# Optimization experiments

Measured on AMD Instinct MI355X. Metric: run time of the kernel, lower is better.

The kernel has to match this reference:

```python
import jax, jax.numpy as jnp
import numpy as np

EPS = 1.1920929e-07  # torch nn.RMSNorm default eps = finfo(fp32).eps
H, NOPE, ROPE, VD = 16, 128, 64, 128
QKD = NOPE + ROPE


def rmsnorm(x, w):
    return x * jax.lax.rsqrt(jnp.mean(x * x, axis=-1, keepdims=True) + EPS) * w


def rope(x, cos, sin):
    # x: [B,S,h,D]; cos/sin broadcast to [B,S,h,D//2]; pairs are (even, odd) interleaved
    x2 = x.reshape(*x.shape[:-1], -1, 2)
    x0, x1 = x2[..., 0], x2[..., 1]
    r = x0 * cos - x1 * sin
    i = x0 * sin + x1 * cos
    return jnp.stack([r, i], axis=-1).reshape(x.shape)


def setup_inputs() -> dict:
    key = jax.random.key(0)
    ks = jax.random.split(key, 8)
    B, S, D = 2, 2048, 2048
    QR, KR = 1536, 512
    x = jax.random.normal(ks[0], (B, S, D), jnp.float32)
    # RoPE table: theta=10000, rope dim 64 -> 32 frequencies
    pos = np.arange(S)[:, None]
    inv = 1.0 / (10000.0 ** (np.arange(0, ROPE, 2) / ROPE))[None, :]
    ang = pos * inv
    freqs_cos = jnp.asarray(np.cos(ang), jnp.float32)
    freqs_sin = jnp.asarray(np.sin(ang), jnp.float32)

    def w(k, out_dim, in_dim):
        return jax.random.normal(k, (out_dim, in_dim), jnp.float32) / np.sqrt(in_dim)

    return {
        "x": x,
        "freqs_cos": freqs_cos,
        "freqs_sin": freqs_sin,
        "Wq_down": w(ks[1], QR, D),
        "q_norm_w": jnp.ones((QR,), jnp.float32),
        "Wq_up": w(ks[2], H * QKD, QR),
        "Wkv_down": w(ks[3], ROPE + KR, D),
        "kv_norm_w": jnp.ones((KR,), jnp.float32),
        "Wkv_up": w(ks[4], H * (VD + NOPE), KR),
        "Wo": w(ks[5], D, H * VD),
        "bo": jnp.zeros((D,), jnp.float32),
        "start_pos": 0,
    }


def reference(x, freqs_cos, freqs_sin, Wq_down, q_norm_w, Wq_up, Wkv_down, kv_norm_w, Wkv_up, Wo, bo, start_pos):
    B, S, D = x.shape
    cos = freqs_cos[None, :, None, :]
    sin = freqs_sin[None, :, None, :]
    # low-rank Q path: down -> RMSNorm -> up
    q = rmsnorm(x @ Wq_down.T, q_norm_w) @ Wq_up.T
    q = q.reshape(B, S, H, QKD)
    q_nope, q_rope = q[..., :NOPE], q[..., NOPE:]
    q_rope = rope(q_rope, cos, sin)
    q = jnp.concatenate([q_nope, q_rope], axis=-1)  # [B,S,H,QKD]
    # low-rank KV path: shared rope part + latent kv
    kv = x @ Wkv_down.T
    k_rope, c_kv = kv[..., :ROPE], kv[..., ROPE:]
    k_rope = rope(k_rope[:, :, None, :], cos, sin)  # [B,S,1,ROPE]
    kv = rmsnorm(c_kv, kv_norm_w) @ Wkv_up.T
    kv = kv.reshape(B, S, H, NOPE + VD)
    k_nope, v = kv[..., :NOPE], kv[..., NOPE:]
    k = jnp.concatenate([k_nope, jnp.broadcast_to(k_rope, (B, S, H, ROPE))], axis=-1)
    # causal SDPA (start_pos=0 prefill: cache slice equals fresh K/V)
    scale = 1.0 / np.sqrt(QKD)
    scores = jnp.einsum("bqhd,bkhd->bhqk", q, k) * scale
    mask = jnp.tril(jnp.ones((S, S), bool))
    scores = jnp.where(mask, scores, -jnp.inf)
    attn = jax.nn.softmax(scores, axis=-1)
    o = jnp.einsum("bhqk,bkhd->bqhd", attn, v).reshape(B, S, H * VD)
    return o @ Wo.T + bo
```

## Files before the change

kernel.cpp:

```cpp
#include <hip/hip_runtime.h>
#include <hip/hip_bf16.h>
#include <stdint.h>


typedef short bf16x8 __attribute__((ext_vector_type(8)));
typedef float f32x4  __attribute__((ext_vector_type(4)));
typedef unsigned int u32;

#define RMS_EPS 1.1920929e-07f
#define SCALE_L2E 0.10411931095f

__device__ __forceinline__ unsigned short f2b(float f) {
  union { float f; uint32_t u; } c; c.f = f;
  uint32_t u = c.u;
  return (unsigned short)((u + 0x7FFFu + ((u >> 16) & 1u)) >> 16);
}
__device__ __forceinline__ float b2f(short s) {
  union { uint32_t u; float f; } c; c.u = ((uint32_t)(unsigned short)s) << 16;
  return c.f;
}
__device__ __forceinline__ u32 pk2(float a, float b) {
  union { __hip_bfloat162 h; u32 u; } cv;
  cv.h = __float22bfloat162_rn(float2{a, b});
  return cv.u;
}
__device__ __forceinline__ void gld16(const short* g, short* l) {
  __builtin_amdgcn_global_load_lds(
      (const __attribute__((address_space(1))) u32*)g,
      (__attribute__((address_space(3))) u32*)l, 16, 0, 0);
}

__global__ void f2bf_kernel(const float* __restrict__ in, short* __restrict__ out, int n4) {
  int i = blockIdx.x * 256 + threadIdx.x;
  if (i >= n4) return;
  float4 v = ((const float4*)in)[i];
  union { ushort4 s; uint2 u; } o;
  o.s.x = f2b(v.x); o.s.y = f2b(v.y); o.s.z = f2b(v.z); o.s.w = f2b(v.w);
  ((uint2*)out)[i] = o.u;
}

__global__ void f2bf_pad_kernel(const float* __restrict__ in, short* __restrict__ out,
                                int n4, int cols4, int src_rows) {
  int i = blockIdx.x * 256 + threadIdx.x;
  if (i >= n4) return;
  int row = i / cols4;
  ushort4 s = {0, 0, 0, 0};
  if (row < src_rows) {
    float4 v = ((const float4*)in)[i];
    s.x = f2b(v.x); s.y = f2b(v.y); s.z = f2b(v.z); s.w = f2b(v.w);
  }
  union { ushort4 ss; uint2 u; } o; o.ss = s;
  ((uint2*)out)[i] = o.u;
}

template <int EPI>
__global__ __launch_bounds__(256) void gemm_bt(
    const short* __restrict__ A, const short* __restrict__ Bt,
    void* __restrict__ Cv, const float* __restrict__ bias,
    int K, int ldc,
    const float* __restrict__ fc, const float* __restrict__ fs,
    short* __restrict__ aux) {
  __shared__ __align__(16) short As[128 * 32];
  __shared__ __align__(16) short Bs[128 * 32];
  int nx = gridDim.x;
  int lin = blockIdx.y * nx + blockIdx.x;
  int cpx = (nx * gridDim.y) >> 3;
  int swz = (lin & 7) * cpx + (lin >> 3);
  int row0 = (swz / nx) * 128, col0 = (swz % nx) * 128;
  int t = threadIdx.x, lane = t & 63, w = t >> 6;
  int wm = w >> 1, wn = w & 1;
  int l15 = lane & 15, l4 = lane >> 4;
  f32x4 acc[4][4] = {};

  int srow = lane >> 2, scol = (lane & 3) * 8;
  const short* Ag = A + (size_t)(row0 + srow) * K + scol;
  const short* Bg = Bt + (size_t)(col0 + srow) * K + scol;

  for (int kt = 0; kt < K; kt += 32) {
#pragma unroll
    for (int c = 0; c < 2; ++c) {
      int blk = w * 2 + c;
      gld16(Ag + (size_t)(blk * 16) * K + kt, As + blk * 512);
      gld16(Bg + (size_t)(blk * 16) * K + kt, Bs + blk * 512);
    }
    __syncthreads();
    bf16x8 af[4], bfr[4];
#pragma unroll
    for (int i = 0; i < 4; ++i) {
      af[i]  = *(const bf16x8*)(As + (wm * 64 + i * 16 + l15) * 32 + l4 * 8);
      bfr[i] = *(const bf16x8*)(Bs + (wn * 64 + i * 16 + l15) * 32 + l4 * 8);
    }
#pragma unroll
    for (int i = 0; i < 4; ++i)
#pragma unroll
      for (int j = 0; j < 4; ++j)
        acc[i][j] = __builtin_amdgcn_mfma_f32_16x16x32_bf16(af[i], bfr[j], acc[i][j], 0, 0, 0);
    __syncthreads();
  }

  if constexpr (EPI == 0) {
    float* C = (float*)Cv;
#pragma unroll
    for (int j = 0; j < 4; ++j) {
      int col = col0 + wn * 64 + j * 16 + l15;
      float bv = bias ? bias[col] : 0.0f;
#pragma unroll
      for (int i = 0; i < 4; ++i) {
        int row = row0 + wm * 64 + i * 16 + l4 * 4;
        float* dst = C + (size_t)row * ldc + col;
#pragma unroll
        for (int r = 0; r < 4; ++r) dst[(size_t)r * ldc] = acc[i][j][r] + bv;
      }
    }
  } else if constexpr (EPI == 1) {
    short* C = (short*)Cv;
#pragma unroll
    for (int j = 0; j < 4; ++j) {
      int col = col0 + wn * 64 + j * 16 + l15;
#pragma unroll
      for (int i = 0; i < 4; ++i) {
        int row = row0 + wm * 64 + i * 16 + l4 * 4;
        short* dst = C + (size_t)row * ldc + col;
#pragma unroll
        for (int r = 0; r < 4; ++r) dst[(size_t)r * ldc] = (short)f2b(acc[i][j][r]);
      }
    }
  } else if constexpr (EPI == 2) {
    short* qb = (short*)Cv;
#pragma unroll
    for (int j = 0; j < 4; ++j) {
      int col = col0 + wn * 64 + j * 16 + l15;
      int h = col / 192;
      int d = col - h * 192;
      bool ro = (d >= 128);
      int ir = ro ? ((d - 128) >> 1) : 0;
      bool odd = (l15 & 1);
#pragma unroll
      for (int i = 0; i < 4; ++i) {
        int rowb = row0 + wm * 64 + i * 16 + l4 * 4;
#pragma unroll
        for (int r = 0; r < 4; ++r) {
          int row = rowb + r;
          int b = row >> 11, s = row & 2047;
          float v = acc[i][j][r];
          float pv = __shfl_xor(v, 1);
          float o;
          if (ro) {
            float c = fc[s * 32 + ir], sn = fs[s * 32 + ir];
            o = odd ? (pv * sn + v * c) : (v * c - pv * sn);
          } else {
            o = v;
          }
          qb[((size_t)((b * 16 + h) * 2048 + s)) * 192 + d] = (short)f2b(o * SCALE_L2E);
        }
      }
    }
  } else {
    short* kb = (short*)Cv;
    short* vT = aux;
    int h = col0 >> 8;
    if ((col0 & 128) == 0) {
#pragma unroll
      for (int j = 0; j < 4; ++j) {
        int d = wn * 64 + j * 16 + l15;
#pragma unroll
        for (int i = 0; i < 4; ++i) {
          int rowb = row0 + wm * 64 + i * 16 + l4 * 4;
#pragma unroll
          for (int r = 0; r < 4; ++r) {
            int row = rowb + r;
            int b = row >> 11, s = row & 2047;
            kb[((size_t)((b * 16 + h) * 2048 + s)) * 192 + d] = (short)f2b(acc[i][j][r]);
          }
        }
      }
    } else {
#pragma unroll
      for (int j = 0; j < 4; ++j) {
        int dv = wn * 64 + j * 16 + l15;
#pragma unroll
        for (int i = 0; i < 4; ++i) {
          int s0 = row0 + wm * 64 + i * 16 + l4 * 4;
          int b = s0 >> 11, s = s0 & 2047;
          short4 o;
          o.x = (short)f2b(acc[i][j][0]);
          o.y = (short)f2b(acc[i][j][1]);
          o.z = (short)f2b(acc[i][j][2]);
          o.w = (short)f2b(acc[i][j][3]);
          *(short4*)(vT + ((size_t)((b * 16 + h) * 128 + dv)) * 2048 + s) = o;
        }
      }
    }
  }
}

template <int W>
__global__ __launch_bounds__(256) void rmsnorm_wave(
    const short* __restrict__ in, const float* __restrict__ wgt,
    short* __restrict__ out, int ld_in) {
  constexpr int NC = W / 512;
  int row = blockIdx.x * 4 + (threadIdx.x >> 6);
  int lane = threadIdx.x & 63;
  const short* x = in + (size_t)row * ld_in + lane * 8;
  float vals[NC * 8];
  float ss = 0.f;
#pragma unroll
  for (int c = 0; c < NC; ++c) {
    bf16x8 v = *(const bf16x8*)(x + c * 512);
#pragma unroll
    for (int k = 0; k < 8; ++k) {
      float f = b2f(v[k]);
      vals[c * 8 + k] = f; ss += f * f;
    }
  }
#pragma unroll
  for (int off = 32; off > 0; off >>= 1) ss += __shfl_xor(ss, off);
  float rs = rsqrtf(ss / (float)W + RMS_EPS);
  short* o = out + (size_t)row * W + lane * 8;
#pragma unroll
  for (int c = 0; c < NC; ++c) {
    const float4* wp = (const float4*)(wgt + c * 512 + lane * 8);
    float4 w0 = wp[0], w1 = wp[1];
    ushort4 lo, hi;
    lo.x = f2b(vals[c * 8 + 0] * rs * w0.x);
    lo.y = f2b(vals[c * 8 + 1] * rs * w0.y);
    lo.z = f2b(vals[c * 8 + 2] * rs * w0.z);
    lo.w = f2b(vals[c * 8 + 3] * rs * w0.w);
    hi.x = f2b(vals[c * 8 + 4] * rs * w1.x);
    hi.y = f2b(vals[c * 8 + 5] * rs * w1.y);
    hi.z = f2b(vals[c * 8 + 6] * rs * w1.z);
    hi.w = f2b(vals[c * 8 + 7] * rs * w1.w);
    *(ushort4*)(o + c * 512) = lo;
    *(ushort4*)(o + c * 512 + 4) = hi;
  }
}

__global__ void prep_krope_kernel(const short* __restrict__ c1,
                                  const float* __restrict__ fc,
                                  const float* __restrict__ fs,
                                  short* __restrict__ kb) {
  int idx = blockIdx.x * 256 + threadIdx.x;
  int i = idx & 31;
  int s = (idx >> 5) & 2047;
  int b = idx >> 16;
  const short* row = c1 + (size_t)(b * 2048 + s) * 2176 + 1536 + 2 * i;
  float x0 = b2f(row[0]), x1 = b2f(row[1]);
  float c = fc[s * 32 + i], sn = fs[s * 32 + i];
  uint32_t pk = (uint32_t)f2b(x0 * c - x1 * sn) | ((uint32_t)f2b(x0 * sn + x1 * c) << 16);
  size_t base = ((size_t)(b * 16) * 2048 + s) * 192 + 128 + 2 * i;
#pragma unroll
  for (int h = 0; h < 16; ++h)
    *(uint32_t*)(kb + base + (size_t)h * 2048 * 192) = pk;
}

__global__ __launch_bounds__(256) void attn_kernel(
    const short* __restrict__ qb, const short* __restrict__ kb,
    const short* __restrict__ vtb, short* __restrict__ ob) {
  __shared__ __align__(16) short Ks[64 * 200];
  __shared__ __align__(16) short Vs[128 * 72];
  int bid = blockIdx.x;
  int xcd = bid & 7, kk2 = bid >> 3;
  int bh = xcd * 4 + (kk2 >> 4);
  int qx = kk2 & 15;
  int b = bh >> 4, h = bh & 15;
  int t = threadIdx.x, lane = t & 63, w = t >> 6;
  int l15 = lane & 15, l4 = lane >> 4;
  const short* Kbh = kb + (size_t)bh * 2048 * 192;
  const short* Vbh = vtb + (size_t)bh * 128 * 2048;

  int sA = (l15 + ((l4 & 1) << 5)) << 2;
  int sB = sA + (16 << 2);
  bool chi = (l4 >> 1) != 0;

  for (int half = 0; half < 2; ++half) {
    int qt = half ? (31 - qx) : qx;
    int q0 = qt * 64;
    const short* Qbase = qb + ((size_t)bh * 2048 + q0 + w * 16) * 192;
    bf16x8 qf[6];
#pragma unroll
    for (int kk = 0; kk < 6; ++kk)
      qf[kk] = *(const bf16x8*)(Qbase + (size_t)l15 * 192 + kk * 32 + l4 * 8);
    f32x4 oaccT[8] = {};
    float m_i = -1e30f, l_i = 0.f;
    int qcol = q0 + w * 16 + l15;
    int kend = q0 + 64;

    for (int kt = 0; kt < kend; kt += 64) {
#pragma unroll
      for (int c = 0; c < 6; ++c) {
        int idx = t + 256 * c;
        int r = idx / 24, ch = idx - r * 24;
        *(bf16x8*)(Ks + r * 200 + ch * 8) =
            *(const bf16x8*)(Kbh + (size_t)(kt + r) * 192 + ch * 8);
      }
#pragma unroll
      for (int c = 0; c < 4; ++c) {
        int idx = t + 256 * c;
        int d = idx >> 3, cc = (idx & 7) * 8;
        *(bf16x8*)(Vs + d * 72 + cc) =
            *(const bf16x8*)(Vbh + (size_t)d * 2048 + kt + cc);
      }
      __syncthreads();

      f32x4 s[4] = {};
      __builtin_amdgcn_s_setprio(1);
#pragma unroll
      for (int kk = 0; kk < 6; ++kk) {
#pragma unroll
        for (int c = 0; c < 4; ++c) {
          bf16x8 kf = *(const bf16x8*)(Ks + (c * 16 + l15) * 200 + kk * 32 + l4 * 8);
          s[c] = __builtin_amdgcn_mfma_f32_16x16x32_bf16(kf, qf[kk], s[c], 0, 0, 0);
        }
      }
      __builtin_amdgcn_s_setprio(0);

      if (kt == q0) {
#pragma unroll
        for (int c = 0; c < 4; ++c)
#pragma unroll
          for (int r = 0; r < 4; ++r) {
            int k = kt + c * 16 + l4 * 4 + r;
            if (k > qcol) s[c][r] = -1e30f;
          }
      }
      float mx = fmaxf(fmaxf(fmaxf(s[0][0], s[0][1]), fmaxf(s[0][2], s[0][3])),
                       fmaxf(fmaxf(s[1][0], s[1][1]), fmaxf(s[1][2], s[1][3])));
      mx = fmaxf(mx, fmaxf(fmaxf(fmaxf(s[2][0], s[2][1]), fmaxf(s[2][2], s[2][3])),
                           fmaxf(fmaxf(s[3][0], s[3][1]), fmaxf(s[3][2], s[3][3]))));
      mx = fmaxf(mx, __shfl_xor(mx, 16));
      mx = fmaxf(mx, __shfl_xor(mx, 32));
      float newm = fmaxf(m_i, mx);
      float alpha = __builtin_amdgcn_exp2f(m_i - newm);
      float rs = 0.f;
#pragma unroll
      for (int c = 0; c < 4; ++c)
#pragma unroll
        for (int r = 0; r < 4; ++r) {
          float p = __builtin_amdgcn_exp2f(s[c][r] - newm);
          s[c][r] = p; rs += p;
        }
      rs += __shfl_xor(rs, 16);
      rs += __shfl_xor(rs, 32);
      l_i = l_i * alpha + rs;
      m_i = newm;
#pragma unroll
      for (int dt = 0; dt < 8; ++dt)
#pragma unroll
        for (int r = 0; r < 4; ++r) oaccT[dt][r] *= alpha;

      u32 pk00 = pk2(s[0][0], s[0][1]), pk01 = pk2(s[0][2], s[0][3]);
      u32 pk10 = pk2(s[1][0], s[1][1]), pk11 = pk2(s[1][2], s[1][3]);
      u32 pk20 = pk2(s[2][0], s[2][1]), pk21 = pk2(s[2][2], s[2][3]);
      u32 pk30 = pk2(s[3][0], s[3][1]), pk31 = pk2(s[3][2], s[3][3]);
      union { bf16x8 v; u32 u[4]; } P0, P1;
      {
        u32 a0 = __builtin_amdgcn_ds_bpermute(sA, (int)pk00);
        u32 a1 = __builtin_amdgcn_ds_bpermute(sA, (int)pk01);
        u32 a2 = __builtin_amdgcn_ds_bpermute(sB, (int)pk00);
        u32 a3 = __builtin_amdgcn_ds_bpermute(sB, (int)pk01);
        u32 b0 = __builtin_amdgcn_ds_bpermute(sA, (int)pk10);
        u32 b1 = __builtin_amdgcn_ds_bpermute(sA, (int)pk11);
        u32 b2 = __builtin_amdgcn_ds_bpermute(sB, (int)pk10);
        u32 b3 = __builtin_amdgcn_ds_bpermute(sB, (int)pk11);
        P0.u[0] = chi ? b0 : a0; P0.u[1] = chi ? b1 : a1;
        P0.u[2] = chi ? b2 : a2; P0.u[3] = chi ? b3 : a3;
      }
      {
        u32 a0 = __builtin_amdgcn_ds_bpermute(sA, (int)pk20);
        u32 a1 = __builtin_amdgcn_ds_bpermute(sA, (int)pk21);
        u32 a2 = __builtin_amdgcn_ds_bpermute(sB, (int)pk20);
        u32 a3 = __builtin_amdgcn_ds_bpermute(sB, (int)pk21);
        u32 b0 = __builtin_amdgcn_ds_bpermute(sA, (int)pk30);
        u32 b1 = __builtin_amdgcn_ds_bpermute(sA, (int)pk31);
        u32 b2 = __builtin_amdgcn_ds_bpermute(sB, (int)pk30);
        u32 b3 = __builtin_amdgcn_ds_bpermute(sB, (int)pk31);
        P1.u[0] = chi ? b0 : a0; P1.u[1] = chi ? b1 : a1;
        P1.u[2] = chi ? b2 : a2; P1.u[3] = chi ? b3 : a3;
      }

      __builtin_amdgcn_s_setprio(1);
#pragma unroll
      for (int dt = 0; dt < 8; ++dt) {
        bf16x8 vf0 = *(const bf16x8*)(Vs + (dt * 16 + l15) * 72 + l4 * 8);
        bf16x8 vf1 = *(const bf16x8*)(Vs + (dt * 16 + l15) * 72 + 32 + l4 * 8);
        oaccT[dt] = __builtin_amdgcn_mfma_f32_16x16x32_bf16(vf0, P0.v, oaccT[dt], 0, 0, 0);
        oaccT[dt] = __builtin_amdgcn_mfma_f32_16x16x32_bf16(vf1, P1.v, oaccT[dt], 0, 0, 0);
      }
      __builtin_amdgcn_s_setprio(0);
      __syncthreads();
    }
    float inv = 1.0f / l_i;
    short* dst = ob + ((size_t)(b * 2048 + qcol)) * 2048 + h * 128;
#pragma unroll
    for (int dt = 0; dt < 8; ++dt) {
      uint2 o;
      o.x = pk2(oaccT[dt][0] * inv, oaccT[dt][1] * inv);
      o.y = pk2(oaccT[dt][2] * inv, oaccT[dt][3] * inv);
      *(uint2*)(dst + dt * 16 + l4 * 4) = o;
    }
  }
}

extern "C" void kernel_launch(void* const* d_in, const int* in_sizes, int n_in,
                              void* d_out, int out_size, void* d_ws, size_t ws_size,
                              hipStream_t stream) {
  const float* x    = (const float*)d_in[0];
  const float* fcos = (const float*)d_in[1];
  const float* fsin = (const float*)d_in[2];
  const float* Wqd  = (const float*)d_in[3];
  const float* qnw  = (const float*)d_in[4];
  const float* Wqu  = (const float*)d_in[5];
  const float* Wkvd = (const float*)d_in[6];
  const float* kvnw = (const float*)d_in[7];
  const float* Wkvu = (const float*)d_in[8];
  const float* Wo   = (const float*)d_in[9];
  const float* bo   = (const float*)d_in[10];
  float* out = (float*)d_out;
  char* ws = (char*)d_ws;

  short* x_bf  = (short*)(ws + 0);
  short* w_cat = (short*)(ws + 16777216);
  short* w_qu  = (short*)(ws + 25690112);
  short* w_kvu = (short*)(ws + 35127296);
  short* w_o   = (short*)(ws + 39321600);
  short* c1    = (short*)(ws + 47710208);
  short* qn    = (short*)(ws + 65536000);
  short* ckvn  = (short*)(ws + 78118912);
  short* q_b   = (short*)(ws + 82313216);
  short* k_b   = (short*)(ws + 107479040);
  short* vT    = (short*)(ws + 132644864);
  short* o_bf  = (short*)(ws + 149422080);

  f2bf_kernel<<<8192, 256, 0, stream>>>(x, x_bf, 2097152);
  f2bf_kernel<<<3072, 256, 0, stream>>>(Wqd, w_cat, 786432);
  f2bf_pad_kernel<<<1280, 256, 0, stream>>>(Wkvd, w_cat + 1536 * 2048, 327680, 512, 576);
  f2bf_kernel<<<4608, 256, 0, stream>>>(Wqu, w_qu, 1179648);
  f2bf_kernel<<<2048, 256, 0, stream>>>(Wkvu, w_kvu, 524288);
  f2bf_kernel<<<4096, 256, 0, stream>>>(Wo, w_o, 1048576);

  gemm_bt<1><<<dim3(17, 32), 256, 0, stream>>>(x_bf, w_cat, c1, nullptr, 2048, 2176,
                                               nullptr, nullptr, nullptr);
  prep_krope_kernel<<<512, 256, 0, stream>>>(c1, fcos, fsin, k_b);
  rmsnorm_wave<1536><<<1024, 256, 0, stream>>>(c1, qnw, qn, 2176);
  rmsnorm_wave<512><<<1024, 256, 0, stream>>>(c1 + 1600, kvnw, ckvn, 2176);

  gemm_bt<2><<<dim3(24, 32), 256, 0, stream>>>(qn, w_qu, q_b, nullptr, 1536, 0,
                                               fcos, fsin, nullptr);
  gemm_bt<3><<<dim3(32, 32), 256, 0, stream>>>(ckvn, w_kvu, k_b, nullptr, 512, 0,
                                               nullptr, nullptr, vT);

  attn_kernel<<<512, 256, 0, stream>>>(q_b, k_b, vT, o_bf);

  gemm_bt<0><<<dim3(16, 32), 256, 0, stream>>>(o_bf, w_o, out, bo, 2048, 2048,
                                               nullptr, nullptr, nullptr);
}
```

Measured before the change: 357.9 us.

## Fuse fp32-to-bf16 conversions, store shared k_rope once, split attention blocks

All six fp32-to-bf16 conversion launches are merged into one kernel. The rope half of K is no longer broadcast into all 16 heads: it is stored once per batch/position and gathered into LDS inside attention, which removes 15/16 of the k_rope writes and shrinks K to 128 columns per head. Attention now launches one block per query tile (1024 blocks) in descending causal-work order instead of pairing two tiles per block. LDS row padding also changes, from 200 to 196 and from 72 to 70. That may alter bank conflicts or the alignment of the 16-byte LDS accesses.

```diff
diff --git a/kernel.cpp b/kernel.cpp
--- a/kernel.cpp
+++ b/kernel.cpp
@@ -30,27 +30,41 @@
       (__attribute__((address_space(3))) u32*)l, 16, 0, 0);
 }
 
-__global__ void f2bf_kernel(const float* __restrict__ in, short* __restrict__ out, int n4) {
-  int i = blockIdx.x * 256 + threadIdx.x;
-  if (i >= n4) return;
+__device__ __forceinline__ void cvt4(const float* __restrict__ in,
+                                     short* __restrict__ out, int i) {
   float4 v = ((const float4*)in)[i];
   union { ushort4 s; uint2 u; } o;
   o.s.x = f2b(v.x); o.s.y = f2b(v.y); o.s.z = f2b(v.z); o.s.w = f2b(v.w);
   ((uint2*)out)[i] = o.u;
 }
 
-__global__ void f2bf_pad_kernel(const float* __restrict__ in, short* __restrict__ out,
-                                int n4, int cols4, int src_rows) {
+__global__ void f2bf_all_kernel(
+    const float* __restrict__ x,    short* __restrict__ x_bf,
+    const float* __restrict__ Wqd,  short* __restrict__ w_qd,
+    const float* __restrict__ Wqu,  short* __restrict__ w_qu,
+    const float* __restrict__ Wkvu, short* __restrict__ w_kvu,
+    const float* __restrict__ Wo,   short* __restrict__ w_o,
+    const float* __restrict__ Wkvd, short* __restrict__ w_kvd) {
   int i = blockIdx.x * 256 + threadIdx.x;
-  if (i >= n4) return;
-  int row = i / cols4;
+  if (i < 2097152) { cvt4(x, x_bf, i); return; }
+  i -= 2097152;
+  if (i < 786432) { cvt4(Wqd, w_qd, i); return; }
+  i -= 786432;
+  if (i < 1179648) { cvt4(Wqu, w_qu, i); return; }
+  i -= 1179648;
+  if (i < 524288) { cvt4(Wkvu, w_kvu, i); return; }
+  i -= 524288;
+  if (i < 1048576) { cvt4(Wo, w_o, i); return; }
+  i -= 1048576;
+  if (i >= 327680) return;
+  int row = i >> 9;
   ushort4 s = {0, 0, 0, 0};
-  if (row < src_rows) {
-    float4 v = ((const float4*)in)[i];
+  if (row < 576) {
+    float4 v = ((const float4*)Wkvd)[i];
     s.x = f2b(v.x); s.y = f2b(v.y); s.z = f2b(v.z); s.w = f2b(v.w);
   }
   union { ushort4 ss; uint2 u; } o; o.ss = s;
-  ((uint2*)out)[i] = o.u;
+  ((uint2*)w_kvd)[i] = o.u;
 }
 
 template <int EPI>
@@ -170,7 +184,7 @@
           for (int r = 0; r < 4; ++r) {
             int row = rowb + r;
             int b = row >> 11, s = row & 2047;
-            kb[((size_t)((b * 16 + h) * 2048 + s)) * 192 + d] = (short)f2b(acc[i][j][r]);
+            kb[((size_t)((b * 16 + h) * 2048 + s)) * 128 + d] = (short)f2b(acc[i][j][r]);
           }
         }
       }
@@ -238,7 +252,7 @@
 __global__ void prep_krope_kernel(const short* __restrict__ c1,
                                   const float* __restrict__ fc,
                                   const float* __restrict__ fs,
-                                  short* __restrict__ kb) {
+                                  short* __restrict__ kr) {
   int idx = blockIdx.x * 256 + threadIdx.x;
   int i = idx & 31;
   int s = (idx >> 5) & 2047;
@@ -247,157 +261,155 @@
   float x0 = b2f(row[0]), x1 = b2f(row[1]);
   float c = fc[s * 32 + i], sn = fs[s * 32 + i];
   uint32_t pk = (uint32_t)f2b(x0 * c - x1 * sn) | ((uint32_t)f2b(x0 * sn + x1 * c) << 16);
-  size_t base = ((size_t)(b * 16) * 2048 + s) * 192 + 128 + 2 * i;
-#pragma unroll
-  for (int h = 0; h < 16; ++h)
-    *(uint32_t*)(kb + base + (size_t)h * 2048 * 192) = pk;
+  *(uint32_t*)(kr + ((size_t)(b * 2048 + s)) * 64 + 2 * i) = pk;
 }
 
 __global__ __launch_bounds__(256) void attn_kernel(
     const short* __restrict__ qb, const short* __restrict__ kb,
-    const short* __restrict__ vtb, short* __restrict__ ob) {
-  __shared__ __align__(16) short Ks[64 * 200];
-  __shared__ __align__(16) short Vs[128 * 72];
+    const short* __restrict__ kr, const short* __restrict__ vtb,
+    short* __restrict__ ob) {
+  __shared__ __align__(16) short Ks[64 * 196];
+  __shared__ __align__(16) short Vs[128 * 70];
   int bid = blockIdx.x;
-  int xcd = bid & 7, kk2 = bid >> 3;
-  int bh = xcd * 4 + (kk2 >> 4);
-  int qx = kk2 & 15;
+  int xcd = bid & 7, rest = bid >> 3;
+  int bh = xcd * 4 + (rest >> 5);
+  int qt = 31 - (rest & 31);
   int b = bh >> 4, h = bh & 15;
   int t = threadIdx.x, lane = t & 63, w = t >> 6;
   int l15 = lane & 15, l4 = lane >> 4;
-  const short* Kbh = kb + (size_t)bh * 2048 * 192;
+  const short* Kbh = kb + (size_t)bh * 2048 * 128;
+  const short* krb = kr + (size_t)b * 2048 * 64;
   const short* Vbh = vtb + (size_t)bh * 128 * 2048;
 
   int sA = (l15 + ((l4 & 1) << 5)) << 2;
   int sB = sA + (16 << 2);
   bool chi = (l4 >> 1) != 0;
 
-  for (int half = 0; half < 2; ++half) {
-    int qt = half ? (31 - qx) : qx;
-    int q0 = qt * 64;
-    const short* Qbase = qb + ((size_t)bh * 2048 + q0 + w * 16) * 192;
-    bf16x8 qf[6];
-#pragma unroll
-    for (int kk = 0; kk < 6; ++kk)
-      qf[kk] = *(const bf16x8*)(Qbase + (size_t)l15 * 192 + kk * 32 + l4 * 8);
-    f32x4 oaccT[8] = {};
-    float m_i = -1e30f, l_i = 0.f;
-    int qcol = q0 + w * 16 + l15;
-    int kend = q0 + 64;
-
-    for (int kt = 0; kt < kend; kt += 64) {
-#pragma unroll
-      for (int c = 0; c < 6; ++c) {
-        int idx = t + 256 * c;
-        int r = idx / 24, ch = idx - r * 24;
-        *(bf16x8*)(Ks + r * 200 + ch * 8) =
-            *(const bf16x8*)(Kbh + (size_t)(kt + r) * 192 + ch * 8);
-      }
+  int q0 = qt * 64;
+  const short* Qbase = qb + ((size_t)bh * 2048 + q0 + w * 16) * 192;
+  bf16x8 qf[6];
+#pragma unroll
+  for (int kk = 0; kk < 6; ++kk)
+    qf[kk] = *(const bf16x8*)(Qbase + (size_t)l15 * 192 + kk * 32 + l4 * 8);
+  f32x4 oaccT[8] = {};
+  float m_i = -1e30f, l_i = 0.f;
+  int qcol = q0 + w * 16 + l15;
+  int kend = q0 + 64;
+
+  for (int kt = 0; kt < kend; kt += 64) {
+#pragma unroll
+    for (int c = 0; c < 6; ++c) {
+      int idx = t + 256 * c;
+      int r = idx / 24, ch = idx - r * 24;
+      const short* src = (ch < 16)
+          ? Kbh + (size_t)(kt + r) * 128 + ch * 8
+          : krb + (size_t)(kt + r) * 64 + (ch - 16) * 8;
+      *(bf16x8*)(Ks + r * 196 + ch * 8) = *(const bf16x8*)src;
+    }
+#pragma unroll
+    for (int c = 0; c < 4; ++c) {
+      int idx = t + 256 * c;
+      int d = idx >> 3, cc = (idx & 7) * 8;
+      *(bf16x8*)(Vs + d * 70 + cc) =
+          *(const bf16x8*)(Vbh + (size_t)d * 2048 + kt + cc);
+    }
+    __syncthreads();
+
+    f32x4 s[4] = {};
+    __builtin_amdgcn_s_setprio(1);
+#pragma unroll
+    for (int kk = 0; kk < 6; ++kk) {
 #pragma unroll
       for (int c = 0; c < 4; ++c) {
-        int idx = t + 256 * c;
-        int d = idx >> 3, cc = (idx & 7) * 8;
-        *(bf16x8*)(Vs + d * 72 + cc) =
-            *(const bf16x8*)(Vbh + (size_t)d * 2048 + kt + cc);
-      }
-      __syncthreads();
-
-      f32x4 s[4] = {};
-      __builtin_amdgcn_s_setprio(1);
-#pragma unroll
-      for (int kk = 0; kk < 6; ++kk) {
-#pragma unroll
-        for (int c = 0; c < 4; ++c) {
-          bf16x8 kf = *(const bf16x8*)(Ks + (c * 16 + l15) * 200 + kk * 32 + l4 * 8);
-          s[c] = __builtin_amdgcn_mfma_f32_16x16x32_bf16(kf, qf[kk], s[c], 0, 0, 0);
+        bf16x8 kf = *(const bf16x8*)(Ks + (c * 16 + l15) * 196 + kk * 32 + l4 * 8);
+        s[c] = __builtin_amdgcn_mfma_f32_16x16x32_bf16(kf, qf[kk], s[c], 0, 0, 0);
+      }
+    }
+    __builtin_amdgcn_s_setprio(0);
+
+    if (kt == q0) {
+#pragma unroll
+      for (int c = 0; c < 4; ++c)
+#pragma unroll
+        for (int r = 0; r < 4; ++r) {
+          int k = kt + c * 16 + l4 * 4 + r;
+          if (k > qcol) s[c][r] = -1e30f;
         }
-      }
-      __builtin_amdgcn_s_setprio(0);
-
-      if (kt == q0) {
-#pragma unroll
-        for (int c = 0; c < 4; ++c)
-#pragma unroll
-          for (int r = 0; r < 4; ++r) {
-            int k = kt + c * 16 + l4 * 4 + r;
-            if (k > qcol) s[c][r] = -1e30f;
-          }
-      }
-      float mx = fmaxf(fmaxf(fmaxf(s[0][0], s[0][1]), fmaxf(s[0][2], s[0][3])),
-                       fmaxf(fmaxf(s[1][0], s[1][1]), fmaxf(s[1][2], s[1][3])));
-      mx = fmaxf(mx, fmaxf(fmaxf(fmaxf(s[2][0], s[2][1]), fmaxf(s[2][2], s[2][3])),
-                           fmaxf(fmaxf(s[3][0], s[3][1]), fmaxf(s[3][2], s[3][3]))));
-      mx = fmaxf(mx, __shfl_xor(mx, 16));
-      mx = fmaxf(mx, __shfl_xor(mx, 32));
-      float newm = fmaxf(m_i, mx);
-      float alpha = __builtin_amdgcn_exp2f(m_i - newm);
-      float rs = 0.f;
-#pragma unroll
-      for (int c = 0; c < 4; ++c)
-#pragma unroll
-        for (int r = 0; r < 4; ++r) {
-          float p = __builtin_amdgcn_exp2f(s[c][r] - newm);
-          s[c][r] = p; rs += p;
-        }
-      rs += __shfl_xor(rs, 16);
-      rs += __shfl_xor(rs, 32);
-      l_i = l_i * alpha + rs;
-      m_i = newm;
-#pragma unroll
-      for (int dt = 0; dt < 8; ++dt)
-#pragma unroll
-        for (int r = 0; r < 4; ++r) oaccT[dt][r] *= alpha;
-
-      u32 pk00 = pk2(s[0][0], s[0][1]), pk01 = pk2(s[0][2], s[0][3]);
-      u32 pk10 = pk2(s[1][0], s[1][1]), pk11 = pk2(s[1][2], s[1][3]);
-      u32 pk20 = pk2(s[2][0], s[2][1]), pk21 = pk2(s[2][2], s[2][3]);
-      u32 pk30 = pk2(s[3][0], s[3][1]), pk31 = pk2(s[3][2], s[3][3]);
-      union { bf16x8 v; u32 u[4]; } P0, P1;
-      {
-        u32 a0 = __builtin_amdgcn_ds_bpermute(sA, (int)pk00);
-        u32 a1 = __builtin_amdgcn_ds_bpermute(sA, (int)pk01);
-        u32 a2 = __builtin_amdgcn_ds_bpermute(sB, (int)pk00);
-        u32 a3 = __builtin_amdgcn_ds_bpermute(sB, (int)pk01);
-        u32 b0 = __builtin_amdgcn_ds_bpermute(sA, (int)pk10);
-        u32 b1 = __builtin_amdgcn_ds_bpermute(sA, (int)pk11);
-        u32 b2 = __builtin_amdgcn_ds_bpermute(sB, (int)pk10);
-        u32 b3 = __builtin_amdgcn_ds_bpermute(sB, (int)pk11);
-        P0.u[0] = chi ? b0 : a0; P0.u[1] = chi ? b1 : a1;
-        P0.u[2] = chi ? b2 : a2; P0.u[3] = chi ? b3 : a3;
-      }
-      {
-        u32 a0 = __builtin_amdgcn_ds_bpermute(sA, (int)pk20);
-        u32 a1 = __builtin_amdgcn_ds_bpermute(sA, (int)pk21);
-        u32 a2 = __builtin_amdgcn_ds_bpermute(sB, (int)pk20);
-        u32 a3 = __builtin_amdgcn_ds_bpermute(sB, (int)pk21);
-        u32 b0 = __builtin_amdgcn_ds_bpermute(sA, (int)pk30);
-        u32 b1 = __builtin_amdgcn_ds_bpermute(sA, (int)pk31);
-        u32 b2 = __builtin_amdgcn_ds_bpermute(sB, (int)pk30);
-        u32 b3 = __builtin_amdgcn_ds_bpermute(sB, (int)pk31);
-        P1.u[0] = chi ? b0 : a0; P1.u[1] = chi ? b1 : a1;
-        P1.u[2] = chi ? b2 : a2; P1.u[3] = chi ? b3 : a3;
-      }
-
-      __builtin_amdgcn_s_setprio(1);
-#pragma unroll
-      for (int dt = 0; dt < 8; ++dt) {
-        bf16x8 vf0 = *(const bf16x8*)(Vs + (dt * 16 + l15) * 72 + l4 * 8);
-        bf16x8 vf1 = *(const bf16x8*)(Vs + (dt * 16 + l15) * 72 + 32 + l4 * 8);
-        oaccT[dt] = __builtin_amdgcn_mfma_f32_16x16x32_bf16(vf0, P0.v, oaccT[dt], 0, 0, 0);
-        oaccT[dt] = __builtin_amdgcn_mfma_f32_16x16x32_bf16(vf1, P1.v, oaccT[dt], 0, 0, 0);
-      }
-      __builtin_amdgcn_s_setprio(0);
-      __syncthreads();
-    }
-    float inv = 1.0f / l_i;
-    short* dst = ob + ((size_t)(b * 2048 + qcol)) * 2048 + h * 128;
+    }
+    float mx = fmaxf(fmaxf(fmaxf(s[0][0], s[0][1]), fmaxf(s[0][2], s[0][3])),
+                     fmaxf(fmaxf(s[1][0], s[1][1]), fmaxf(s[1][2], s[1][3])));
+    mx = fmaxf(mx, fmaxf(fmaxf(fmaxf(s[2][0], s[2][1]), fmaxf(s[2][2], s[2][3])),
+                         fmaxf(fmaxf(s[3][0], s[3][1]), fmaxf(s[3][2], s[3][3]))));
+    mx = fmaxf(mx, __shfl_xor(mx, 16));
+    mx = fmaxf(mx, __shfl_xor(mx, 32));
+    float newm = fmaxf(m_i, mx);
+    float alpha = __builtin_amdgcn_exp2f(m_i - newm);
+    float rs = 0.f;
+#pragma unroll
+    for (int c = 0; c < 4; ++c)
+#pragma unroll
+      for (int r = 0; r < 4; ++r) {
+        float p = __builtin_amdgcn_exp2f(s[c][r] - newm);
+        s[c][r] = p; rs += p;
+      }
+    rs += __shfl_xor(rs, 16);
+    rs += __shfl_xor(rs, 32);
+    l_i = l_i * alpha + rs;
+    m_i = newm;
+#pragma unroll
+    for (int dt = 0; dt < 8; ++dt)
+#pragma unroll
+      for (int r = 0; r < 4; ++r) oaccT[dt][r] *= alpha;
+
+    u32 pk00 = pk2(s[0][0], s[0][1]), pk01 = pk2(s[0][2], s[0][3]);
+    u32 pk10 = pk2(s[1][0], s[1][1]), pk11 = pk2(s[1][2], s[1][3]);
+    u32 pk20 = pk2(s[2][0], s[2][1]), pk21 = pk2(s[2][2], s[2][3]);
+    u32 pk30 = pk2(s[3][0], s[3][1]), pk31 = pk2(s[3][2], s[3][3]);
+    union { bf16x8 v; u32 u[4]; } P0, P1;
+    {
+      u32 a0 = __builtin_amdgcn_ds_bpermute(sA, (int)pk00);
+      u32 a1 = __builtin_amdgcn_ds_bpermute(sA, (int)pk01);
+      u32 a2 = __builtin_amdgcn_ds_bpermute(sB, (int)pk00);
+      u32 a3 = __builtin_amdgcn_ds_bpermute(sB, (int)pk01);
+      u32 b0 = __builtin_amdgcn_ds_bpermute(sA, (int)pk10);
+      u32 b1 = __builtin_amdgcn_ds_bpermute(sA, (int)pk11);
+      u32 b2 = __builtin_amdgcn_ds_bpermute(sB, (int)pk10);
+      u32 b3 = __builtin_amdgcn_ds_bpermute(sB, (int)pk11);
+      P0.u[0] = chi ? b0 : a0; P0.u[1] = chi ? b1 : a1;
+      P0.u[2] = chi ? b2 : a2; P0.u[3] = chi ? b3 : a3;
+    }
+    {
+      u32 a0 = __builtin_amdgcn_ds_bpermute(sA, (int)pk20);
+      u32 a1 = __builtin_amdgcn_ds_bpermute(sA, (int)pk21);
+      u32 a2 = __builtin_amdgcn_ds_bpermute(sB, (int)pk20);
+      u32 a3 = __builtin_amdgcn_ds_bpermute(sB, (int)pk21);
+      u32 b0 = __builtin_amdgcn_ds_bpermute(sA, (int)pk30);
+      u32 b1 = __builtin_amdgcn_ds_bpermute(sA, (int)pk31);
+      u32 b2 = __builtin_amdgcn_ds_bpermute(sB, (int)pk30);
+      u32 b3 = __builtin_amdgcn_ds_bpermute(sB, (int)pk31);
+      P1.u[0] = chi ? b0 : a0; P1.u[1] = chi ? b1 : a1;
+      P1.u[2] = chi ? b2 : a2; P1.u[3] = chi ? b3 : a3;
+    }
+
+    __builtin_amdgcn_s_setprio(1);
 #pragma unroll
     for (int dt = 0; dt < 8; ++dt) {
-      uint2 o;
-      o.x = pk2(oaccT[dt][0] * inv, oaccT[dt][1] * inv);
-      o.y = pk2(oaccT[dt][2] * inv, oaccT[dt][3] * inv);
-      *(uint2*)(dst + dt * 16 + l4 * 4) = o;
-    }
+      bf16x8 vf0 = *(const bf16x8*)(Vs + (dt * 16 + l15) * 70 + l4 * 8);
+      bf16x8 vf1 = *(const bf16x8*)(Vs + (dt * 16 + l15) * 70 + 32 + l4 * 8);
+      oaccT[dt] = __builtin_amdgcn_mfma_f32_16x16x32_bf16(vf0, P0.v, oaccT[dt], 0, 0, 0);
+      oaccT[dt] = __builtin_amdgcn_mfma_f32_16x16x32_bf16(vf1, P1.v, oaccT[dt], 0, 0, 0);
+    }
+    __builtin_amdgcn_s_setprio(0);
+    __syncthreads();
+  }
+  float inv = 1.0f / l_i;
+  short* dst = ob + ((size_t)(b * 2048 + qcol)) * 2048 + h * 128;
+#pragma unroll
+  for (int dt = 0; dt < 8; ++dt) {
+    uint2 o;
+    o.x = pk2(oaccT[dt][0] * inv, oaccT[dt][1] * inv);
+    o.y = pk2(oaccT[dt][2] * inv, oaccT[dt][3] * inv);
+    *(uint2*)(dst + dt * 16 + l4 * 4) = o;
   }
 }
 
@@ -430,17 +442,15 @@
   short* k_b   = (short*)(ws + 107479040);
   short* vT    = (short*)(ws + 132644864);
   short* o_bf  = (short*)(ws + 149422080);
-
-  f2bf_kernel<<<8192, 256, 0, stream>>>(x, x_bf, 2097152);
-  f2bf_kernel<<<3072, 256, 0, stream>>>(Wqd, w_cat, 786432);
-  f2bf_pad_kernel<<<1280, 256, 0, stream>>>(Wkvd, w_cat + 1536 * 2048, 327680, 512, 576);
-  f2bf_kernel<<<4608, 256, 0, stream>>>(Wqu, w_qu, 1179648);
-  f2bf_kernel<<<2048, 256, 0, stream>>>(Wkvu, w_kvu, 524288);
-  f2bf_kernel<<<4096, 256, 0, stream>>>(Wo, w_o, 1048576);
+  short* kr    = (short*)(ws + 166199296);
+
+  f2bf_all_kernel<<<23296, 256, 0, stream>>>(x, x_bf, Wqd, w_cat, Wqu, w_qu,
+                                             Wkvu, w_kvu, Wo, w_o,
+                                             Wkvd, w_cat + 1536 * 2048);
 
   gemm_bt<1><<<dim3(17, 32), 256, 0, stream>>>(x_bf, w_cat, c1, nullptr, 2048, 2176,
                                                nullptr, nullptr, nullptr);
-  prep_krope_kernel<<<512, 256, 0, stream>>>(c1, fcos, fsin, k_b);
+  prep_krope_kernel<<<512, 256, 0, stream>>>(c1, fcos, fsin, kr);
   rmsnorm_wave<1536><<<1024, 256, 0, stream>>>(c1, qnw, qn, 2176);
   rmsnorm_wave<512><<<1024, 256, 0, stream>>>(c1 + 1600, kvnw, ckvn, 2176);
 
@@ -449,7 +459,7 @@
   gemm_bt<3><<<dim3(32, 32), 256, 0, stream>>>(ckvn, w_kvu, k_b, nullptr, 512, 0,
                                                nullptr, nullptr, vT);
 
-  attn_kernel<<<512, 256, 0, stream>>>(q_b, k_b, vT, o_bf);
+  attn_kernel<<<1024, 256, 0, stream>>>(q_b, k_b, kr, vT, o_bf);
 
   gemm_bt<0><<<dim3(16, 32), 256, 0, stream>>>(o_bf, w_o, out, bo, 2048, 2048,
                                                nullptr, nullptr, nullptr);
```

Result: slower. 389.9 us (+9.0%).
